# Kernel optimization log

Measured on AMD Instinct MI355X. Metric: run time of the kernel, lower is better.

## Reference

```python
import jax, jax.numpy as jnp
import numpy as np

N_NODES = 100000
N_EDGES = 3200000
IN_F, HID, NC = 384, 64, 2


def setup_inputs() -> dict:
    key = jax.random.key(0)
    ks = jax.random.split(key, 8)
    X = jax.random.normal(ks[0], (N_NODES, IN_F), dtype=jnp.float32)
    edge_index = jax.random.randint(ks[1], (2, N_EDGES), 0, N_NODES, dtype=jnp.int64)
    edge_weight = jax.random.uniform(ks[2], (N_EDGES,), dtype=jnp.float32)
    W1 = jax.random.normal(ks[3], (IN_F, HID), dtype=jnp.float32) / np.sqrt(IN_F)
    b1 = jnp.zeros((HID,), dtype=jnp.float32)
    W2 = jax.random.normal(ks[4], (HID, HID), dtype=jnp.float32) / np.sqrt(HID)
    b2 = jnp.zeros((HID,), dtype=jnp.float32)
    Wm1 = jax.random.normal(ks[5], (HID, HID), dtype=jnp.float32) / np.sqrt(HID)
    bm1 = jnp.zeros((HID,), dtype=jnp.float32)
    Wm2 = jax.random.normal(ks[6], (HID, NC), dtype=jnp.float32) / np.sqrt(HID)
    bm2 = jnp.zeros((NC,), dtype=jnp.float32)
    return {"X": X, "edge_index": edge_index, "edge_weight": edge_weight,
            "W1": W1, "b1": b1, "W2": W2, "b2": b2,
            "Wm1": Wm1, "bm1": bm1, "Wm2": Wm2, "bm2": bm2}


def _gcn_norm(edge_index, edge_weight, n):
    # add self-loops with weight 1 (PyG gcn_norm, add_self_loops=True)
    loop = jnp.arange(n, dtype=edge_index.dtype)
    row = jnp.concatenate([edge_index[0], loop])
    col = jnp.concatenate([edge_index[1], loop])
    w = jnp.concatenate([edge_weight, jnp.ones((n,), edge_weight.dtype)])
    deg = jax.ops.segment_sum(w, col, num_segments=n)
    dis = jnp.where(deg > 0, jax.lax.rsqrt(jnp.where(deg > 0, deg, 1.0)), 0.0)
    norm = dis[row] * w * dis[col]  # [E+N]
    return row, col, norm


def _gcn_conv(x, row, col, norm, W, b, n):
    h = x @ W                                   # [N, out]
    msg = norm[:, None] * h[row]                # gather + scale  [E+N, out]
    return jax.ops.segment_sum(msg, col, num_segments=n) + b


def reference(X, edge_index, edge_weight, W1, b1, W2, b2, Wm1, bm1, Wm2, bm2):
    n = X.shape[0]
    row, col, norm = _gcn_norm(edge_index, edge_weight, n)
    # PyG BasicGNN: act (leaky_relu) after all but last conv; dropout off in eval
    h = _gcn_conv(X, row, col, norm, W1, b1, n)
    h = jax.nn.leaky_relu(h, negative_slope=0.01)
    h = _gcn_conv(h, row, col, norm, W2, b2, n)
    # MLP: Linear -> Dropout(eval: identity) -> ELU -> Linear
    h = jax.nn.elu(h @ Wm1 + bm1)
    logits = h @ Wm2 + bm2
    return jax.nn.softmax(logits, axis=-1)
```

## Files before the change

kernel.cpp:

```cpp
#include <hip/hip_runtime.h>
#include <math.h>

#define NN 100000
#define NE 3200000
#define INF 384
#define HID 64
#define CAP 48
#define OVF_CAP 65536
#define NBIN 391
#define NREP 8
#define NCTR (NBIN * NREP)
#define SCAN_VPT 13
#define EPB 8192
#define NBLK ((NE + EPB - 1) / EPB)

typedef unsigned long long ulong64;
typedef unsigned int uint32;
typedef unsigned short ushort16;
typedef __attribute__((ext_vector_type(8))) short bf16x8;
typedef __attribute__((ext_vector_type(4))) float f32x4;

__device__ inline float bf16_to_f(uint32 us) { return __uint_as_float(us << 16); }
__device__ inline ushort16 f_to_bf16(float f) {
    uint32 u = __float_as_uint(f);
    u += 0x7FFF + ((u >> 16) & 1);
    return (ushort16)(u >> 16);
}
__device__ inline void split_bf16(float x, ushort16& h, ushort16& l) {
    h = f_to_bf16(x);
    float hf = bf16_to_f((uint32)h);
    l = f_to_bf16(x - hf);
}


__global__ void init_kernel(int* __restrict__ ovf_cnt, int* __restrict__ bincnt) {
    int i = blockIdx.x * blockDim.x + threadIdx.x;
    if (i < NCTR) bincnt[i] = 0;
    if (i == 0) *ovf_cnt = 0;
}


__global__ __launch_bounds__(256) void wprep_kernel(const float* __restrict__ W1,
                                                    const float* __restrict__ W2,
                                                    const float* __restrict__ Wm1,
                                                    ushort16* __restrict__ wp1h,
                                                    ushort16* __restrict__ wp1l,
                                                    ushort16* __restrict__ wp2h,
                                                    ushort16* __restrict__ wp2l,
                                                    ushort16* __restrict__ wpm1h,
                                                    ushort16* __restrict__ wpm1l) {
    int i = blockIdx.x * blockDim.x + threadIdx.x;
    int np = gridDim.x * blockDim.x;
    for (int idx = i; idx < INF * HID; idx += np) {
        int k = idx >> 6, j = idx & 63;
        ushort16 h, l;
        split_bf16(W1[idx], h, l);
        size_t dst = ((size_t)(((k >> 5) * 4 + (j >> 4)) * 64 +
                               ((j & 15) | (((k >> 3) & 3) << 4))) << 3) + (k & 7);
        wp1h[dst] = h;
        wp1l[dst] = l;
    }
    for (int idx = i; idx < HID * HID; idx += np) {
        int k = idx >> 6, j = idx & 63;
        size_t dst = ((size_t)(((k >> 5) * 4 + (j >> 4)) * 64 +
                               ((j & 15) | (((k >> 3) & 3) << 4))) << 3) + (k & 7);
        ushort16 h, l;
        split_bf16(W2[idx], h, l);
        wp2h[dst] = h;
        wp2l[dst] = l;
        split_bf16(Wm1[idx], h, l);
        wpm1h[dst] = h;
        wpm1l[dst] = l;
    }
}


__global__ __launch_bounds__(1024) void binhist_kernel(const int* __restrict__ col,
                                                       int* __restrict__ bincnt) {
    __shared__ int h[NBIN];
    if (threadIdx.x < NBIN) h[threadIdx.x] = 0;
    __syncthreads();
    int rep = blockIdx.x & (NREP - 1);
    int base = blockIdx.x * EPB;
#pragma unroll
    for (int i = 0; i < 8; i++) {
        int e = base + i * 1024 + threadIdx.x;
        if (e < NE) atomicAdd(&h[col[e] >> 8], 1);
    }
    __syncthreads();
    if (threadIdx.x < NBIN && h[threadIdx.x] > 0)
        atomicAdd(&bincnt[threadIdx.x * NREP + rep], h[threadIdx.x]);
}


__global__ __launch_bounds__(256) void binscan_kernel(const int* __restrict__ bincnt,
                                                      int* __restrict__ binbase,
                                                      int* __restrict__ bincur) {
    __shared__ int tot[256];
    int t = threadIdx.x;
    int v[SCAN_VPT];
    int s = 0;
#pragma unroll
    for (int i = 0; i < SCAN_VPT; i++) {
        int idx = t * SCAN_VPT + i;
        v[i] = (idx < NCTR) ? bincnt[idx] : 0;
        s += v[i];
    }
    tot[t] = s;
    __syncthreads();
    for (int off = 1; off < 256; off <<= 1) {
        int x = (t >= off) ? tot[t - off] : 0;
        __syncthreads();
        tot[t] += x;
        __syncthreads();
    }
    int run = tot[t] - s;
#pragma unroll
    for (int i = 0; i < SCAN_VPT; i++) {
        int idx = t * SCAN_VPT + i;
        if (idx < NCTR) { binbase[idx] = run; bincur[idx] = run; }
        run += v[i];
    }
    if (t == 255) binbase[NCTR] = NE;
}


__global__ __launch_bounds__(1024) void binscatter_kernel(const int* __restrict__ row,
                                                          const int* __restrict__ col,
                                                          const float* __restrict__ ew,
                                                          int* __restrict__ bincur,
                                                          ulong64* __restrict__ ebin) {
    __shared__ int lhist[NBIN];
    __shared__ int lbase[NBIN];
    int tid = threadIdx.x;
    int rep = blockIdx.x & (NREP - 1);
    int base = blockIdx.x * EPB;
    if (tid < NBIN) lhist[tid] = 0;
    __syncthreads();
    int brk[8], rr[8];
    uint32 wb[8];
#pragma unroll
    for (int i = 0; i < 8; i++) {
        int e = base + i * 1024 + tid;
        brk[i] = -1;
        if (e < NE) {
            int r = row[e];
            int c = col[e];
            wb[i] = __float_as_uint(ew[e]);
            int b = c >> 8;
            int rk = atomicAdd(&lhist[b], 1);
            brk[i] = (b << 16) | rk;
            rr[i] = r | ((c & 255) << 17);
        }
    }
    __syncthreads();
    if (tid < NBIN && lhist[tid] > 0)
        lbase[tid] = atomicAdd(&bincur[tid * NREP + rep], lhist[tid]);
    __syncthreads();
#pragma unroll
    for (int i = 0; i < 8; i++) {
        if (brk[i] >= 0) {
            int pos = lbase[brk[i] >> 16] + (brk[i] & 0xFFFF);
            ebin[pos] = ((ulong64)wb[i] << 32) | (uint32)rr[i];
        }
    }
}


__global__ __launch_bounds__(256) void bucket_kernel(const int* __restrict__ binbase,
                                                     const ulong64* __restrict__ ebin,
                                                     ulong64* __restrict__ sedge,
                                                     int* __restrict__ cnt,
                                                     float* __restrict__ dis,
                                                     int* __restrict__ ovf_cnt,
                                                     int4* __restrict__ ovf) {
    __shared__ int cur[256];
    __shared__ float sdeg[256];
    int bin = blockIdx.x;
    int node0 = bin << 8;
    cur[threadIdx.x] = 0;
    sdeg[threadIdx.x] = 0.f;
    __syncthreads();
    int start = binbase[bin * NREP];
    int end = binbase[(bin + 1) * NREP];
    for (int i = start + threadIdx.x; i < end; i += 256) {
        ulong64 pk = ebin[i];
        int r = (int)(pk & 0x1FFFF);
        int lc = (int)((pk >> 17) & 255);
        uint32 wb = (uint32)(pk >> 32);
        atomicAdd(&sdeg[lc], __uint_as_float(wb));
        int rank = atomicAdd(&cur[lc], 1);
        int node = node0 + lc;
        if (rank < CAP) {
            sedge[(size_t)node * CAP + rank] = ((ulong64)wb << 32) | (uint32)r;
        } else {
            int o = atomicAdd(ovf_cnt, 1);
            if (o < OVF_CAP) ovf[o] = make_int4(r, node, (int)wb, 0);
        }
    }
    __syncthreads();
    int node = node0 + threadIdx.x;
    if (node < NN) {
        cnt[node] = min(cur[threadIdx.x], CAP);
        dis[node] = rsqrtf(sdeg[threadIdx.x] + 1.0f);
    }
}


template <int K, bool LEAKY>
__global__ __launch_bounds__(256, 6) void mfma_gemm_kernel(const float* __restrict__ A,
                                                           const ushort16* __restrict__ Wph,
                                                           const ushort16* __restrict__ Wpl,
                                                           ushort16* __restrict__ out) {
    __shared__ ushort16 Xh[64][72];
    __shared__ ushort16 Xl[64][72];
    const int tid = threadIdx.x;
    const int nb = blockIdx.x * 64;
    const int w = tid >> 6;
    const int l = tid & 63;
    const int lrow = l & 15;
    const int lkb = (l >> 4) * 8;
    const bf16x8* __restrict__ Bh = (const bf16x8*)Wph;
    const bf16x8* __restrict__ Bl = (const bf16x8*)Wpl;

    f32x4 acc[4];
#pragma unroll
    for (int n = 0; n < 4; n++) acc[n] = (f32x4){0.f, 0.f, 0.f, 0.f};

    constexpr int NT = K / 64;
    float4 vreg[4];

#pragma unroll
    for (int t = 0; t < 4; t++) {
        int f = t * 256 + tid;
        int rr = f >> 4;
        int c4 = f & 15;
        int gr = nb + rr;
        vreg[t] = make_float4(0.f, 0.f, 0.f, 0.f);
        if (gr < NN) vreg[t] = *(const float4*)&A[(size_t)gr * K + c4 * 4];
    }

#pragma unroll
    for (int kt = 0; kt < NT; kt++) {
#pragma unroll
        for (int t = 0; t < 4; t++) {
            int f = t * 256 + tid;
            int rr = f >> 4;
            int c4 = f & 15;
            float4 v = vreg[t];
            if (LEAKY) {
                v.x = v.x > 0.f ? v.x : 0.01f * v.x;
                v.y = v.y > 0.f ? v.y : 0.01f * v.y;
                v.z = v.z > 0.f ? v.z : 0.01f * v.z;
                v.w = v.w > 0.f ? v.w : 0.01f * v.w;
            }
            ushort4 oh, ol;
            split_bf16(v.x, oh.x, ol.x);
            split_bf16(v.y, oh.y, ol.y);
            split_bf16(v.z, oh.z, ol.z);
            split_bf16(v.w, oh.w, ol.w);
            *(ushort4*)&Xh[rr][c4 * 4] = oh;
            *(ushort4*)&Xl[rr][c4 * 4] = ol;
        }
        __syncthreads();
        if (kt + 1 < NT) {
#pragma unroll
            for (int t = 0; t < 4; t++) {
                int f = t * 256 + tid;
                int rr = f >> 4;
                int c4 = f & 15;
                int gr = nb + rr;
                vreg[t] = make_float4(0.f, 0.f, 0.f, 0.f);
                if (gr < NN)
                    vreg[t] = *(const float4*)&A[(size_t)gr * K + (kt + 1) * 64 + c4 * 4];
            }
        }
#pragma unroll
        for (int ks = 0; ks < 2; ks++) {
            int ktl = ks * 32 + lkb;
            int kslot = kt * 2 + ks;
            bf16x8 ah = *(const bf16x8*)&Xh[w * 16 + lrow][ktl];
            bf16x8 al = *(const bf16x8*)&Xl[w * 16 + lrow][ktl];
#pragma unroll
            for (int n = 0; n < 4; n++) {
                bf16x8 bh = Bh[(size_t)(kslot * 4 + n) * 64 + l];
                bf16x8 bl = Bl[(size_t)(kslot * 4 + n) * 64 + l];
                acc[n] = __builtin_amdgcn_mfma_f32_16x16x32_bf16(ah, bh, acc[n], 0, 0, 0);
                acc[n] = __builtin_amdgcn_mfma_f32_16x16x32_bf16(al, bh, acc[n], 0, 0, 0);
                acc[n] = __builtin_amdgcn_mfma_f32_16x16x32_bf16(ah, bl, acc[n], 0, 0, 0);
            }
        }
        __syncthreads();
    }
    int rbase = nb + w * 16 + (l >> 4) * 4;
#pragma unroll
    for (int r = 0; r < 4; r++) {
        int node = rbase + r;
        if (node < NN) {
#pragma unroll
            for (int n = 0; n < 4; n++)
                out[(size_t)node * HID + n * 16 + lrow] = f_to_bf16(acc[n][r]);
        }
    }
}


__global__ __launch_bounds__(256) void aggregate_kernel(const int* __restrict__ cnt,
                                                        const ulong64* __restrict__ sedge,
                                                        const float* __restrict__ dis,
                                                        const ushort16* __restrict__ h,
                                                        const float* __restrict__ bias,
                                                        float* __restrict__ out) {
    int lane = threadIdx.x & 63;
    int n = blockIdx.x * 4 + (threadIdx.x >> 6);
    if (n >= NN) return;
    int c = cnt[n];
    ulong64 pk = 0;
    if (lane < c) pk = sedge[(size_t)n * CAP + lane];
    int r_l = (int)(uint32)pk;
    float w_l = __uint_as_float((uint32)(pk >> 32));
    float dn = dis[n];
    float nm_l = w_l * dn * dis[r_l];

    float acc = bias[lane] + dn * dn * bf16_to_f(h[(size_t)n * HID + lane]);
    int j = 0;
    for (; j + 3 < c; j += 4) {
        int r0 = __shfl(r_l, j), r1 = __shfl(r_l, j + 1);
        int r2 = __shfl(r_l, j + 2), r3 = __shfl(r_l, j + 3);
        float w0 = __shfl(nm_l, j), w1 = __shfl(nm_l, j + 1);
        float w2 = __shfl(nm_l, j + 2), w3 = __shfl(nm_l, j + 3);
        float v0 = bf16_to_f(h[(size_t)r0 * HID + lane]);
        float v1 = bf16_to_f(h[(size_t)r1 * HID + lane]);
        float v2 = bf16_to_f(h[(size_t)r2 * HID + lane]);
        float v3 = bf16_to_f(h[(size_t)r3 * HID + lane]);
        acc = fmaf(w0, v0, acc);
        acc = fmaf(w1, v1, acc);
        acc = fmaf(w2, v2, acc);
        acc = fmaf(w3, v3, acc);
    }
    for (; j < c; j++) {
        int rj = __shfl(r_l, j);
        float wj = __shfl(nm_l, j);
        acc = fmaf(wj, bf16_to_f(h[(size_t)rj * HID + lane]), acc);
    }
    out[(size_t)n * HID + lane] = acc;
}


__global__ __launch_bounds__(256) void ovf_kernel(const int* __restrict__ ovf_cnt,
                                                  const int4* __restrict__ ovf,
                                                  const float* __restrict__ dis,
                                                  const ushort16* __restrict__ h,
                                                  float* __restrict__ out) {
    int lane = threadIdx.x & 63;
    int wid = blockIdx.x * 4 + (threadIdx.x >> 6);
    int nw = gridDim.x * 4;
    int c = min(*ovf_cnt, OVF_CAP);
    for (int i = wid; i < c; i += nw) {
        int4 t = ovf[i];
        float w = __int_as_float(t.z);
        float nrm = dis[t.x] * w * dis[t.y];
        atomicAdd(&out[(size_t)t.y * HID + lane],
                  nrm * bf16_to_f(h[(size_t)t.x * HID + lane]));
    }
}


__global__ __launch_bounds__(256) void mlp_mfma_kernel(const float* __restrict__ agg,
                                                       const ushort16* __restrict__ Wph,
                                                       const ushort16* __restrict__ Wpl,
                                                       const float* __restrict__ bm1,
                                                       const float* __restrict__ Wm2,
                                                       const float* __restrict__ bm2,
                                                       float* __restrict__ out) {
    __shared__ ushort16 Xh[64][72];
    __shared__ ushort16 Xl[64][72];
    const int tid = threadIdx.x;
    const int nb = blockIdx.x * 64;
    const int w = tid >> 6;
    const int l = tid & 63;
    const int lrow = l & 15;
    const int lkb = (l >> 4) * 8;
    const bf16x8* __restrict__ Bh = (const bf16x8*)Wph;
    const bf16x8* __restrict__ Bl = (const bf16x8*)Wpl;

#pragma unroll
    for (int t = 0; t < 4; t++) {
        int f = t * 256 + tid;
        int rr = f >> 4;
        int c4 = f & 15;
        int gr = nb + rr;
        float4 v = make_float4(0.f, 0.f, 0.f, 0.f);
        if (gr < NN) v = *(const float4*)&agg[(size_t)gr * HID + c4 * 4];
        ushort4 oh, ol;
        split_bf16(v.x, oh.x, ol.x);
        split_bf16(v.y, oh.y, ol.y);
        split_bf16(v.z, oh.z, ol.z);
        split_bf16(v.w, oh.w, ol.w);
        *(ushort4*)&Xh[rr][c4 * 4] = oh;
        *(ushort4*)&Xl[rr][c4 * 4] = ol;
    }
    __syncthreads();

    f32x4 acc[4];
#pragma unroll
    for (int n = 0; n < 4; n++) acc[n] = (f32x4){0.f, 0.f, 0.f, 0.f};

#pragma unroll
    for (int ks = 0; ks < 2; ks++) {
        bf16x8 ah = *(const bf16x8*)&Xh[w * 16 + lrow][ks * 32 + lkb];
        bf16x8 al = *(const bf16x8*)&Xl[w * 16 + lrow][ks * 32 + lkb];
#pragma unroll
        for (int n = 0; n < 4; n++) {
            bf16x8 bh = Bh[(size_t)(ks * 4 + n) * 64 + l];
            bf16x8 bl = Bl[(size_t)(ks * 4 + n) * 64 + l];
            acc[n] = __builtin_amdgcn_mfma_f32_16x16x32_bf16(ah, bh, acc[n], 0, 0, 0);
            acc[n] = __builtin_amdgcn_mfma_f32_16x16x32_bf16(al, bh, acc[n], 0, 0, 0);
            acc[n] = __builtin_amdgcn_mfma_f32_16x16x32_bf16(ah, bl, acc[n], 0, 0, 0);
        }
    }

    float b1c[4], w2a[4], w2b[4];
#pragma unroll
    for (int n = 0; n < 4; n++) {
        int colw = n * 16 + lrow;
        b1c[n] = bm1[colw];
        w2a[n] = Wm2[colw * 2];
        w2b[n] = Wm2[colw * 2 + 1];
    }
    float b20 = bm2[0], b21 = bm2[1];

#pragma unroll
    for (int r = 0; r < 4; r++) {
        float s0 = 0.f, s1 = 0.f;
#pragma unroll
        for (int n = 0; n < 4; n++) {
            float u = acc[n][r] + b1c[n];
            u = u > 0.f ? u : (expf(u) - 1.f);
            s0 = fmaf(u, w2a[n], s0);
            s1 = fmaf(u, w2b[n], s1);
        }
#pragma unroll
        for (int off = 1; off < 16; off <<= 1) {
            s0 += __shfl_xor(s0, off);
            s1 += __shfl_xor(s1, off);
        }
        int node = nb + w * 16 + (l >> 4) * 4 + r;
        if (lrow == 0 && node < NN) {
            float l0 = s0 + b20, l1 = s1 + b21;
            float m = fmaxf(l0, l1);
            float e0 = expf(l0 - m), e1 = expf(l1 - m);
            float inv = 1.f / (e0 + e1);
            *(float2*)&out[(size_t)node * 2] = make_float2(e0 * inv, e1 * inv);
        }
    }
}


extern "C" void kernel_launch(void* const* d_in, const int* in_sizes, int n_in,
                              void* d_out, int out_size, void* d_ws, size_t ws_size,
                              hipStream_t stream) {
    const float* X   = (const float*)d_in[0];
    const int*   ei  = (const int*)d_in[1];
    const float* ew  = (const float*)d_in[2];
    const float* W1  = (const float*)d_in[3];
    const float* b1  = (const float*)d_in[4];
    const float* W2  = (const float*)d_in[5];
    const float* b2  = (const float*)d_in[6];
    const float* Wm1 = (const float*)d_in[7];
    const float* bm1 = (const float*)d_in[8];
    const float* Wm2 = (const float*)d_in[9];
    const float* bm2 = (const float*)d_in[10];
    const int* row = ei;
    const int* col = ei + NE;
    float* out = (float*)d_out;

    const size_t MB = 1024 * 1024;
    const size_t KB = 1024;
    char* ws = (char*)d_ws;
    float*    dis     = (float*)   (ws + 0 * MB);
    int*      cnt     = (int*)     (ws + 1 * MB);
    ushort16* wp1h    = (ushort16*)(ws + 2 * MB);
    ushort16* wp1l    = (ushort16*)(ws + 2 * MB + 64 * KB);
    ushort16* wp2h    = (ushort16*)(ws + 2 * MB + 128 * KB);
    ushort16* wp2l    = (ushort16*)(ws + 2 * MB + 144 * KB);
    ushort16* wpm1h   = (ushort16*)(ws + 2 * MB + 160 * KB);
    ushort16* wpm1l   = (ushort16*)(ws + 2 * MB + 176 * KB);
    int*      ovf_cnt = (int*)     (ws + 3 * MB);
    int*      binbase = (int*)     (ws + 3 * MB + 4 * KB);
    int*      bincur  = (int*)     (ws + 3 * MB + 20 * KB);
    int*      bincnt  = (int*)     (ws + 3 * MB + 36 * KB);
    int4*     ovf     = (int4*)    (ws + 4 * MB);
    ulong64*  ebin    = (ulong64*) (ws + 5 * MB);
    float*    h2      = (float*)   (ws + 5 * MB);
    ulong64*  sedge   = (ulong64*) (ws + 31 * MB);
    ushort16* h1      = (ushort16*)(ws + 70 * MB);

    init_kernel<<<(NCTR + 255) / 256, 256, 0, stream>>>(ovf_cnt, bincnt);
    wprep_kernel<<<64, 256, 0, stream>>>(W1, W2, Wm1, wp1h, wp1l, wp2h, wp2l, wpm1h, wpm1l);
    binhist_kernel<<<NBLK, 1024, 0, stream>>>(col, bincnt);
    binscan_kernel<<<1, 256, 0, stream>>>(bincnt, binbase, bincur);
    binscatter_kernel<<<NBLK, 1024, 0, stream>>>(row, col, ew, bincur, ebin);
    bucket_kernel<<<NBIN, 256, 0, stream>>>(binbase, ebin, sedge, cnt, dis, ovf_cnt, ovf);

    mfma_gemm_kernel<INF, false><<<(NN + 63) / 64, 256, 0, stream>>>(X, wp1h, wp1l, h1);
    aggregate_kernel<<<(NN + 3) / 4, 256, 0, stream>>>(cnt, sedge, dis, h1, b1, h2);
    ovf_kernel<<<256, 256, 0, stream>>>(ovf_cnt, ovf, dis, h1, h2);

    mfma_gemm_kernel<HID, true><<<(NN + 63) / 64, 256, 0, stream>>>(h2, wp2h, wp2l, h1);
    aggregate_kernel<<<(NN + 3) / 4, 256, 0, stream>>>(cnt, sedge, dis, h1, b2, h2);
    ovf_kernel<<<256, 256, 0, stream>>>(ovf_cnt, ovf, dis, h1, h2);

    mlp_mfma_kernel<<<(NN + 63) / 64, 256, 0, stream>>>(h2, wpm1h, wpm1l, bm1, Wm2, bm2, out);
}
```

Baseline: 551.8 us.

## Fold source-side degree norm into GEMM output and batch edge loads in aggregation

The GEMM epilogue now multiplies each output row by dis[node], so aggregation no longer has to gather dis[row] per edge. The output is scaled by dn once at the end, and the self-loop term becomes the pre-scaled hs[n]. Each node's edge list is zero-padded to a multiple of 8 so the aggregate loop reads 8 packed edges per step without bounds checks. It uses uniform (scalar) loads instead of lane shuffles, which exposes more independent gathers. The padding adds extra stores in the bucket kernel and wasted zero-weight gathers of row 0.

New measurement: 513.0 us. 1.08x faster.

```diff
diff --git a/kernel.cpp b/kernel.cpp
--- a/kernel.cpp
+++ b/kernel.cpp
@@ -201,7 +201,10 @@
     __syncthreads();
     int node = node0 + threadIdx.x;
     if (node < NN) {
-        cnt[node] = min(cur[threadIdx.x], CAP);
+        int cc = min(cur[threadIdx.x], CAP);
+        cnt[node] = cc;
+        int cpad = min((cc + 7) & ~7, CAP);
+        for (int s = cc; s < cpad; s++) sedge[(size_t)node * CAP + s] = 0;
         dis[node] = rsqrtf(sdeg[threadIdx.x] + 1.0f);
     }
 }
@@ -211,6 +214,7 @@
 __global__ __launch_bounds__(256, 6) void mfma_gemm_kernel(const float* __restrict__ A,
                                                            const ushort16* __restrict__ Wph,
                                                            const ushort16* __restrict__ Wpl,
+                                                           const float* __restrict__ dis,
                                                            ushort16* __restrict__ out) {
     __shared__ ushort16 Xh[64][72];
     __shared__ ushort16 Xl[64][72];
@@ -297,9 +301,10 @@
     for (int r = 0; r < 4; r++) {
         int node = rbase + r;
         if (node < NN) {
+            float ds = dis[node];
 #pragma unroll
             for (int n = 0; n < 4; n++)
-                out[(size_t)node * HID + n * 16 + lrow] = f_to_bf16(acc[n][r]);
+                out[(size_t)node * HID + n * 16 + lrow] = f_to_bf16(acc[n][r] * ds);
         }
     }
 }
@@ -308,49 +313,41 @@
 __global__ __launch_bounds__(256) void aggregate_kernel(const int* __restrict__ cnt,
                                                         const ulong64* __restrict__ sedge,
                                                         const float* __restrict__ dis,
-                                                        const ushort16* __restrict__ h,
+                                                        const ushort16* __restrict__ hs,
                                                         const float* __restrict__ bias,
                                                         float* __restrict__ out) {
     int lane = threadIdx.x & 63;
-    int n = blockIdx.x * 4 + (threadIdx.x >> 6);
+    int wslot = __builtin_amdgcn_readfirstlane(threadIdx.x >> 6);
+    int n = blockIdx.x * 4 + wslot;
     if (n >= NN) return;
     int c = cnt[n];
-    ulong64 pk = 0;
-    if (lane < c) pk = sedge[(size_t)n * CAP + lane];
-    int r_l = (int)(uint32)pk;
-    float w_l = __uint_as_float((uint32)(pk >> 32));
+    int cpad = (c + 7) & ~7;
     float dn = dis[n];
-    float nm_l = w_l * dn * dis[r_l];
-
-    float acc = bias[lane] + dn * dn * bf16_to_f(h[(size_t)n * HID + lane]);
-    int j = 0;
-    for (; j + 3 < c; j += 4) {
-        int r0 = __shfl(r_l, j), r1 = __shfl(r_l, j + 1);
-        int r2 = __shfl(r_l, j + 2), r3 = __shfl(r_l, j + 3);
-        float w0 = __shfl(nm_l, j), w1 = __shfl(nm_l, j + 1);
-        float w2 = __shfl(nm_l, j + 2), w3 = __shfl(nm_l, j + 3);
-        float v0 = bf16_to_f(h[(size_t)r0 * HID + lane]);
-        float v1 = bf16_to_f(h[(size_t)r1 * HID + lane]);
-        float v2 = bf16_to_f(h[(size_t)r2 * HID + lane]);
-        float v3 = bf16_to_f(h[(size_t)r3 * HID + lane]);
-        acc = fmaf(w0, v0, acc);
-        acc = fmaf(w1, v1, acc);
-        acc = fmaf(w2, v2, acc);
-        acc = fmaf(w3, v3, acc);
-    }
-    for (; j < c; j++) {
-        int rj = __shfl(r_l, j);
-        float wj = __shfl(nm_l, j);
-        acc = fmaf(wj, bf16_to_f(h[(size_t)rj * HID + lane]), acc);
-    }
-    out[(size_t)n * HID + lane] = acc;
+    const ulong64* __restrict__ el = sedge + (size_t)n * CAP;
+
+    float acc = bf16_to_f((uint32)hs[(size_t)n * HID + lane]);
+    for (int j = 0; j < cpad; j += 8) {
+        ulong64 p[8];
+#pragma unroll
+        for (int i = 0; i < 8; i++) p[i] = el[j + i];
+        float v[8], wv[8];
+#pragma unroll
+        for (int i = 0; i < 8; i++) {
+            uint32 r = (uint32)p[i];
+            wv[i] = __uint_as_float((uint32)(p[i] >> 32));
+            v[i] = bf16_to_f((uint32)hs[(size_t)r * HID + lane]);
+        }
+#pragma unroll
+        for (int i = 0; i < 8; i++) acc = fmaf(wv[i], v[i], acc);
+    }
+    out[(size_t)n * HID + lane] = fmaf(dn, acc, bias[lane]);
 }
 
 
 __global__ __launch_bounds__(256) void ovf_kernel(const int* __restrict__ ovf_cnt,
                                                   const int4* __restrict__ ovf,
                                                   const float* __restrict__ dis,
-                                                  const ushort16* __restrict__ h,
+                                                  const ushort16* __restrict__ hs,
                                                   float* __restrict__ out) {
     int lane = threadIdx.x & 63;
     int wid = blockIdx.x * 4 + (threadIdx.x >> 6);
@@ -359,9 +356,9 @@
     for (int i = wid; i < c; i += nw) {
         int4 t = ovf[i];
         float w = __int_as_float(t.z);
-        float nrm = dis[t.x] * w * dis[t.y];
+        float nrm = w * dis[t.y];
         atomicAdd(&out[(size_t)t.y * HID + lane],
-                  nrm * bf16_to_f(h[(size_t)t.x * HID + lane]));
+                  nrm * bf16_to_f((uint32)hs[(size_t)t.x * HID + lane]));
     }
 }
 
@@ -503,11 +500,11 @@
     binscatter_kernel<<<NBLK, 1024, 0, stream>>>(row, col, ew, bincur, ebin);
     bucket_kernel<<<NBIN, 256, 0, stream>>>(binbase, ebin, sedge, cnt, dis, ovf_cnt, ovf);
 
-    mfma_gemm_kernel<INF, false><<<(NN + 63) / 64, 256, 0, stream>>>(X, wp1h, wp1l, h1);
+    mfma_gemm_kernel<INF, false><<<(NN + 63) / 64, 256, 0, stream>>>(X, wp1h, wp1l, dis, h1);
     aggregate_kernel<<<(NN + 3) / 4, 256, 0, stream>>>(cnt, sedge, dis, h1, b1, h2);
     ovf_kernel<<<256, 256, 0, stream>>>(ovf_cnt, ovf, dis, h1, h2);
 
-    mfma_gemm_kernel<HID, true><<<(NN + 63) / 64, 256, 0, stream>>>(h2, wp2h, wp2l, h1);
+    mfma_gemm_kernel<HID, true><<<(NN + 63) / 64, 256, 0, stream>>>(h2, wp2h, wp2l, dis, h1);
     aggregate_kernel<<<(NN + 3) / 4, 256, 0, stream>>>(cnt, sedge, dis, h1, b2, h2);
     ovf_kernel<<<256, 256, 0, stream>>>(ovf_cnt, ovf, dis, h1, h2);
 
```
